# Optimization experiments

Measured on AMD Instinct MI355X. Metric: run time of the kernel, lower is better.

Reference implementation:

```python
import jax, jax.numpy as jnp
import numpy as np

B, S, D = 4, 4096, 256


def _complex_linear(x_r, x_i, w_r, w_i):
    # torch nn.Linear: y = x @ W.T ; complex mult: (Wr + i Wi)(xr + i xi)
    real = x_r @ w_r.T - x_i @ w_i.T
    imag = x_i @ w_r.T + x_r @ w_i.T
    return real, imag


def setup_inputs() -> dict:
    key = jax.random.key(0)
    ks = jax.random.split(key, 8)
    std = 1.0 / np.sqrt(D)  # ~ nn.Linear default init scale
    return {
        "query_real": jax.random.normal(ks[0], (B, S, D), jnp.float32),
        "query_imag": jax.random.normal(ks[1], (B, S, D), jnp.float32),
        "wq_real": jax.random.normal(ks[2], (D, D), jnp.float32) * std,
        "wq_imag": jax.random.normal(ks[3], (D, D), jnp.float32) * std,
        "wk_real": jax.random.normal(ks[4], (D, D), jnp.float32) * std,
        "wk_imag": jax.random.normal(ks[5], (D, D), jnp.float32) * std,
        "wv_real": jax.random.normal(ks[6], (D, D), jnp.float32) * std,
        "wv_imag": jax.random.normal(ks[7], (D, D), jnp.float32) * std,
    }


def reference(query_real, query_imag, wq_real, wq_imag, wk_real, wk_imag, wv_real, wv_imag):
    dim = query_real.shape[-1]
    scale = dim ** (-0.5)  # faithful: uses dim, not 2*dim

    q_r, q_i = _complex_linear(query_real, query_imag, wq_real, wq_imag)
    k_r, k_i = _complex_linear(query_real, query_imag, wk_real, wk_imag)
    v_r, v_i = _complex_linear(query_real, query_imag, wv_real, wv_imag)

    q_flat = jnp.concatenate([q_r, q_i], axis=-1)  # [B,S,2D]
    k_flat = jnp.concatenate([k_r, k_i], axis=-1)  # [B,S,2D]

    scores = jnp.einsum('bqd,bkd->bqk', q_flat, k_flat) * scale  # [B,S,S]
    attn = jax.nn.softmax(scores, axis=-1)

    out_r = jnp.einsum('bqk,bkd->bqd', attn, v_r)
    out_i = jnp.einsum('bqk,bkd->bqd', attn, v_i)
    return out_r, out_i, attn
```

## Files before the change

kernel.cpp:

```cpp
#include <hip/hip_runtime.h>
#include <hip/hip_fp16.h>

typedef _Float16 f16;
typedef _Float16 f16x8 __attribute__((ext_vector_type(8)));
typedef _Float16 f16x4 __attribute__((ext_vector_type(4)));
typedef float f32x4 __attribute__((ext_vector_type(4)));

#define AS1 __attribute__((address_space(1)))
#define AS3 __attribute__((address_space(3)))

__device__ __forceinline__ void g2l16(const void* g, void* l) {
  __builtin_amdgcn_global_load_lds((const AS1 void*)g, (AS3 void*)l, 16, 0, 0);
}

__device__ __forceinline__ void xcd_swz(int& bx, int& by, int& bz) {
  int gx = gridDim.x, gy = gridDim.y;
  int nwg = gx * gy * gridDim.z;
  int lin = (blockIdx.z * gy + blockIdx.y) * gx + blockIdx.x;
  int swz = (lin & 7) * (nwg >> 3) + (lin >> 3);
  bx = swz % gx;
  int t = swz / gx;
  by = t % gy;
  bz = t / gy;
}

__global__ __launch_bounds__(256) void build_x(const float* __restrict__ qr,
                                               const float* __restrict__ qi,
                                               f16* __restrict__ X) {
  long i = (long)blockIdx.x * 256 + threadIdx.x;
  long e = i * 4;
  int m = (int)(e >> 9);
  int k = (int)(e & 511);
  const float* src = (k < 256) ? (qr + (long)m * 256 + k)
                               : (qi + (long)m * 256 + (k - 256));
  float4 v = *(const float4*)src;
  f16x4 h = {(f16)v.x, (f16)v.y, (f16)v.z, (f16)v.w};
  *(f16x4*)(X + e) = h;
}

__global__ __launch_bounds__(256) void build_w(const float* __restrict__ wqr,
                                               const float* __restrict__ wqi,
                                               const float* __restrict__ wkr,
                                               const float* __restrict__ wki,
                                               const float* __restrict__ wvr,
                                               const float* __restrict__ wvi,
                                               f16* __restrict__ W) {
  long i = (long)blockIdx.x * 256 + threadIdx.x;
  long e = i * 4;
  int n = (int)(e >> 9);
  int k = (int)(e & 511);
  int sel = n >> 8;
  int row = n & 255;
  int k2 = k & 255;
  bool hi = (k >= 256);
  const float *Wr, *Wi;
  if ((sel >> 1) == 0)      { Wr = wqr; Wi = wqi; }
  else if ((sel >> 1) == 1) { Wr = wkr; Wi = wki; }
  else                      { Wr = wvr; Wi = wvi; }
  const float* src;
  float sgn = 1.0f;
  if ((sel & 1) == 0) {
    if (!hi) src = Wr + (long)row * 256 + k2;
    else   { src = Wi + (long)row * 256 + k2; sgn = -1.0f; }
  } else {
    if (!hi) src = Wi + (long)row * 256 + k2;
    else     src = Wr + (long)row * 256 + k2;
  }
  float4 v = *(const float4*)src;
  f16x4 h = {(f16)(sgn * v.x), (f16)(sgn * v.y), (f16)(sgn * v.z), (f16)(sgn * v.w)};
  *(f16x4*)(W + e) = h;
}

template <int MODE>
__global__ __launch_bounds__(256) void gemm_nt(const f16* __restrict__ A, int lda, long astr,
                                               const f16* __restrict__ B, int ldb, long bstr,
                                               int K, float scale,
                                               void* __restrict__ C0, long cstr,
                                               float2* __restrict__ stats) {
  __shared__ __align__(16) f16 As[128 * 64];
  __shared__ __align__(16) f16 Bs[128 * 64];
  int bx, by, bz;
  xcd_swz(bx, by, bz);
  const f16* Ab = A + (long)bz * astr;
  const f16* Bb = B + (long)bz * bstr;
  const int tid = threadIdx.x;
  const int wave = tid >> 6, lane = tid & 63;
  const int bm = by * 128, bn = bx * 128;
  const int wm = (wave >> 1) * 64, wn = (wave & 1) * 64;
  const int lr = lane & 15, lg = lane >> 4;

  const int srow = wave * 8 + (lane >> 3);
  const int sk = ((lane & 7) ^ (lane >> 3)) * 8;

  f32x4 acc[4][4] = {};

  for (int kt = 0; kt < K; kt += 64) {
#pragma unroll
    for (int it = 0; it < 4; ++it) {
      int r = srow + it * 32;
      g2l16(Ab + (long)(bm + r) * lda + kt + sk, (char*)As + it * 4096 + wave * 1024);
      g2l16(Bb + (long)(bn + r) * ldb + kt + sk, (char*)Bs + it * 4096 + wave * 1024);
    }
    __syncthreads();
#pragma unroll
    for (int kk = 0; kk < 2; ++kk) {
      f16x8 af[4], bf[4];
#pragma unroll
      for (int f = 0; f < 4; ++f) {
        int sw = ((kk * 4 + lg) ^ (lr & 7)) * 8;
        af[f] = *(const f16x8*)(As + (wm + f * 16 + lr) * 64 + sw);
        bf[f] = *(const f16x8*)(Bs + (wn + f * 16 + lr) * 64 + sw);
      }
#pragma unroll
      for (int fm = 0; fm < 4; ++fm)
#pragma unroll
        for (int fn = 0; fn < 4; ++fn)
          acc[fm][fn] = __builtin_amdgcn_mfma_f32_16x16x32_f16(af[fm], bf[fn], acc[fm][fn], 0, 0, 0);
    }
    __syncthreads();
  }

#pragma unroll
  for (int fm = 0; fm < 4; ++fm) {
#pragma unroll
    for (int fn = 0; fn < 4; ++fn) {
#pragma unroll
      for (int r = 0; r < 4; ++r) {
        int row = bm + wm + fm * 16 + lg * 4 + r;
        int col = bn + wn + fn * 16 + lr;
        float v = acc[fm][fn][r];
        if (MODE == 0) {
          ((f16*)C0)[(long)row * 1536 + col] = (f16)v;
        } else {
          ((f16*)C0)[(long)bz * cstr + (long)row * 4096 + col] = (f16)(v * scale);
        }
      }
    }
  }

  if (MODE == 1) {
    const int nt = bx * 2 + (wn >> 6);
#pragma unroll
    for (int fm = 0; fm < 4; ++fm) {
#pragma unroll
      for (int r = 0; r < 4; ++r) {
        float v0 = acc[fm][0][r] * scale, v1 = acc[fm][1][r] * scale;
        float v2 = acc[fm][2][r] * scale, v3 = acc[fm][3][r] * scale;
        float mt = fmaxf(fmaxf(v0, v1), fmaxf(v2, v3));
#pragma unroll
        for (int off = 8; off >= 1; off >>= 1) mt = fmaxf(mt, __shfl_xor(mt, off));
        float lt = __expf(v0 - mt) + __expf(v1 - mt) + __expf(v2 - mt) + __expf(v3 - mt);
#pragma unroll
        for (int off = 8; off >= 1; off >>= 1) lt += __shfl_xor(lt, off);
        if (lr == 0) {
          int row = bm + wm + fm * 16 + lg * 4 + r;
          stats[(long)nt * 16384 + (long)bz * 4096 + row] = make_float2(mt, lt);
        }
      }
    }
  }
}

__global__ __launch_bounds__(256) void build_vt(const f16* __restrict__ P,
                                                f16* __restrict__ VT) {
  __shared__ f16 t[64][66];
  const int tid = threadIdx.x;
  const long b = blockIdx.z;
  const f16* src = P + (b * 4096 + (long)blockIdx.x * 64) * 1536 + 1024 + blockIdx.y * 64;
#pragma unroll
  for (int it = 0; it < 16; ++it) {
    int lin = it * 256 + tid;
    int i = lin >> 6, j = lin & 63;
    t[i][j] = src[(long)i * 1536 + j];
  }
  __syncthreads();
  f16* dst = VT + (b * 512 + (long)blockIdx.y * 64) * 4096 + blockIdx.x * 64;
#pragma unroll
  for (int it = 0; it < 16; ++it) {
    int lin = it * 256 + tid;
    int i = lin >> 6, j = lin & 63;
    dst[(long)i * 4096 + j] = t[j][i];
  }
}

__global__ __launch_bounds__(256) void merge_stats(const float2* __restrict__ stats,
                                                   float2* __restrict__ ml) {
  long row = (long)blockIdx.x * 256 + threadIdx.x;
  float m = -1e30f;
#pragma unroll 8
  for (int i = 0; i < 64; ++i) m = fmaxf(m, stats[i * 16384 + row].x);
  float l = 0.0f;
#pragma unroll 8
  for (int i = 0; i < 64; ++i) {
    float2 s = stats[i * 16384 + row];
    l += s.y * __expf(s.x - m);
  }
  ml[row] = make_float2(m, l);
}

__global__ __launch_bounds__(512, 4) void pv_fused2(const float2* __restrict__ ml,
                                                    const f16* __restrict__ S16,
                                                    const f16* __restrict__ VT,
                                                    float* __restrict__ attn,
                                                    float* __restrict__ outR,
                                                    float* __restrict__ outI) {
  __shared__ __align__(16) f16 Ps0[64 * 64];
  __shared__ __align__(16) f16 Ps1[64 * 64];
  __shared__ __align__(16) f16 Bs0[256 * 64];
  __shared__ __align__(16) f16 Bs1[256 * 64];
  int lin = blockIdx.x;
  int swz = (lin & 7) * 64 + (lin >> 3);
  int b = swz >> 7;
  int rem = swz & 127;
  int rt = rem >> 1, ch = rem & 1;
  const int bm = rt * 64;
  const int c0 = ch * 256;

  const int tid = threadIdx.x;
  const int wave = tid >> 6, lane = tid & 63;
  const int wm2 = (wave >> 2) * 32;
  const int wn2 = (wave & 3) * 64;
  const int lr = lane & 15, lg = lane >> 4;

  const int prow = tid >> 3;
  const int pc8 = tid & 7;
  const int vrow = wave * 8 + (lane >> 3);
  const int vsw = ((lane & 7) ^ ((lane >> 3) & 7)) * 8;
  float2 mlv = ml[(long)b * 4096 + bm + prow];
  const float mrow = mlv.x;
  const float invl = 1.0f / mlv.y;
  const bool writer = (ch == 0);

  const f16* Sb = S16 + ((long)(b * 4096 + bm + prow)) * 4096 + pc8 * 8;
  float* Ab = attn + ((long)(b * 4096 + bm + prow)) * 4096 + pc8 * 8;
  const f16* Vb = VT + (long)(b * 512 + c0) * 4096;
  const int pslot = (pc8 ^ (prow & 7)) * 8;

  f32x4 acc[2][4] = {};
  f16x8 sc0, sc1;

#define PV_EXP(SC, PSBUF, KT)                                               \
  {                                                                         \
    float p[8];                                                             \
    _Pragma("unroll") for (int j = 0; j < 8; ++j)                           \
      p[j] = __expf((float)SC[j] - mrow) * invl;                            \
    if (writer) {                                                           \
      float4 w0 = {p[0], p[1], p[2], p[3]};                                 \
      float4 w1 = {p[4], p[5], p[6], p[7]};                                 \
      *(float4*)(Ab + (KT)) = w0;                                           \
      *(float4*)(Ab + (KT) + 4) = w1;                                       \
    }                                                                       \
    f16x8 h = {(f16)p[0], (f16)p[1], (f16)p[2], (f16)p[3],                  \
               (f16)p[4], (f16)p[5], (f16)p[6], (f16)p[7]};                 \
    *(f16x8*)(PSBUF + prow * 64 + pslot) = h;                               \
  }

#define PV_MFMA(PSBUF, BSBUF)                                               \
  {                                                                         \
    _Pragma("unroll")                                                       \
    for (int kk = 0; kk < 2; ++kk) {                                        \
      f16x8 af[2];                                                          \
      _Pragma("unroll")                                                     \
      for (int fm = 0; fm < 2; ++fm)                                        \
        af[fm] = *(const f16x8*)(PSBUF + (wm2 + fm * 16 + lr) * 64 +        \
                                 ((kk * 4 + lg) ^ (lr & 7)) * 8);           \
      f16x8 bf[4];                                                          \
      _Pragma("unroll")                                                     \
      for (int f = 0; f < 4; ++f)                                           \
        bf[f] = *(const f16x8*)(BSBUF + (wn2 + f * 16 + lr) * 64 +          \
                                ((kk * 4 + lg) ^ (lr & 7)) * 8);            \
      _Pragma("unroll")                                                     \
      for (int fm = 0; fm < 2; ++fm)                                        \
        _Pragma("unroll")                                                   \
        for (int f = 0; f < 4; ++f)                                         \
          acc[fm][f] = __builtin_amdgcn_mfma_f32_16x16x32_f16(              \
              af[fm], bf[f], acc[fm][f], 0, 0, 0);                          \
    }                                                                       \
  }

#define PV_G2L(BSBUF, KT)                                                   \
  {                                                                         \
    _Pragma("unroll")                                                       \
    for (int i = 0; i < 4; ++i)                                             \
      g2l16(Vb + (long)(i * 64 + vrow) * 4096 + (KT) + vsw,                 \
            (char*)BSBUF + i * 8192 + wave * 1024);                         \
  }

#define PV_STEP(T, SA, SB, PSC, BSC, PSN, BSN)                              \
  {                                                                         \
    if ((T) + 2 < 64) SA = *(const f16x8*)(Sb + ((T) + 2) * 64);            \
    if ((T) + 1 < 64) PV_G2L(BSN, ((T) + 1) * 64)                           \
    PV_MFMA(PSC, BSC)                                                       \
    if ((T) + 1 < 64) PV_EXP(SB, PSN, ((T) + 1) * 64)                       \
    __syncthreads();                                                        \
  }

  sc0 = *(const f16x8*)(Sb + 0);
  sc1 = *(const f16x8*)(Sb + 64);
  PV_G2L(Bs0, 0)
  PV_EXP(sc0, Ps0, 0)
  __syncthreads();

  for (int t2 = 0; t2 < 64; t2 += 2) {
    PV_STEP(t2,     sc0, sc1, Ps0, Bs0, Ps1, Bs1)
    PV_STEP(t2 + 1, sc1, sc0, Ps1, Bs1, Ps0, Bs0)
  }
#undef PV_STEP
#undef PV_G2L
#undef PV_MFMA
#undef PV_EXP

  float* outp = ch ? outI : outR;
#pragma unroll
  for (int fm = 0; fm < 2; ++fm)
#pragma unroll
    for (int f = 0; f < 4; ++f)
#pragma unroll
      for (int r = 0; r < 4; ++r) {
        int row = bm + wm2 + fm * 16 + lg * 4 + r;
        int col = wn2 + f * 16 + lr;
        outp[((long)b * 4096 + row) * 256 + col] = acc[fm][f][r];
      }
}

extern "C" void kernel_launch(void* const* d_in, const int* in_sizes, int n_in,
                              void* d_out, int out_size, void* d_ws, size_t ws_size,
                              hipStream_t stream) {
  const float* qr  = (const float*)d_in[0];
  const float* qi  = (const float*)d_in[1];
  const float* wqr = (const float*)d_in[2];
  const float* wqi = (const float*)d_in[3];
  const float* wkr = (const float*)d_in[4];
  const float* wki = (const float*)d_in[5];
  const float* wvr = (const float*)d_in[6];
  const float* wvi = (const float*)d_in[7];

  float* outR = (float*)d_out;
  float* outI = outR + (size_t)4 * 4096 * 256;
  float* attn = outI + (size_t)4 * 4096 * 256;

  const size_t offX  = 0;
  const size_t offW  = offX + (size_t)16384 * 512 * 2;
  const size_t offP  = offW + (size_t)1536 * 512 * 2;
  const size_t offVT = offP + (size_t)16384 * 1536 * 2;
  const size_t offS  = offVT + (size_t)4 * 512 * 4096 * 2;

  char* ws = (char*)d_ws;
  f16* X   = (f16*)(ws + offX);
  f16* W   = (f16*)(ws + offW);
  f16* P   = (f16*)(ws + offP);
  f16* VT  = (f16*)(ws + offVT);
  f16* S16 = (f16*)(ws + offS);
  float2* stats = (float2*)X;
  float2* ml    = (float2*)W;

  build_x<<<8192, 256, 0, stream>>>(qr, qi, X);
  build_w<<<768, 256, 0, stream>>>(wqr, wqi, wkr, wki, wvr, wvi, W);

  gemm_nt<0><<<dim3(12, 128, 1), 256, 0, stream>>>(X, 512, 0L, W, 512, 0L, 512, 1.0f,
                                                   (void*)P, 0L, nullptr);

  build_vt<<<dim3(64, 8, 4), 256, 0, stream>>>(P, VT);

  gemm_nt<1><<<dim3(32, 32, 4), 256, 0, stream>>>(P, 1536, (long)4096 * 1536,
                                                  P + 512, 1536, (long)4096 * 1536,
                                                  512, 0.0625f,
                                                  (void*)S16, (long)4096 * 4096, stats);

  merge_stats<<<64, 256, 0, stream>>>(stats, ml);

  pv_fused2<<<512, 512, 0, stream>>>(ml, S16, VT, attn, outR, outI);
}
```

Measured before the change: 375.6 us.

## Enlarge GEMM tiles to 256x128 and halve PV k-step for higher occupancy

The NT GEMM kernel now runs 512 threads per block on a 256x128 output tile instead of 256 threads on 128x128. This halves the grid and reuses each loaded B tile across twice as many rows. The fused softmax-PV kernel switches from 64-wide to 32-wide K slices with smaller LDS buffers, a new swizzle and an occupancy hint of 6. The aim is to fit more resident blocks and hide latency, at the cost of twice as many barrier-separated steps and narrower per-thread attn stores.

```diff
diff --git a/kernel.cpp b/kernel.cpp
--- a/kernel.cpp
+++ b/kernel.cpp
@@ -72,12 +72,12 @@
 }
 
 template <int MODE>
-__global__ __launch_bounds__(256) void gemm_nt(const f16* __restrict__ A, int lda, long astr,
-                                               const f16* __restrict__ B, int ldb, long bstr,
-                                               int K, float scale,
-                                               void* __restrict__ C0, long cstr,
-                                               float2* __restrict__ stats) {
-  __shared__ __align__(16) f16 As[128 * 64];
+__global__ __launch_bounds__(512, 4) void gemm_nt(const f16* __restrict__ A, int lda, long astr,
+                                                  const f16* __restrict__ B, int ldb, long bstr,
+                                                  int K, float scale,
+                                                  void* __restrict__ C0, long cstr,
+                                                  float2* __restrict__ stats) {
+  __shared__ __align__(16) f16 As[256 * 64];
   __shared__ __align__(16) f16 Bs[128 * 64];
   int bx, by, bz;
   xcd_swz(bx, by, bz);
@@ -85,7 +85,7 @@
   const f16* Bb = B + (long)bz * bstr;
   const int tid = threadIdx.x;
   const int wave = tid >> 6, lane = tid & 63;
-  const int bm = by * 128, bn = bx * 128;
+  const int bm = by * 256, bn = bx * 128;
   const int wm = (wave >> 1) * 64, wn = (wave & 1) * 64;
   const int lr = lane & 15, lg = lane >> 4;
 
@@ -96,11 +96,13 @@
 
   for (int kt = 0; kt < K; kt += 64) {
 #pragma unroll
-    for (int it = 0; it < 4; ++it) {
-      int r = srow + it * 32;
-      g2l16(Ab + (long)(bm + r) * lda + kt + sk, (char*)As + it * 4096 + wave * 1024);
-      g2l16(Bb + (long)(bn + r) * ldb + kt + sk, (char*)Bs + it * 4096 + wave * 1024);
-    }
+    for (int it = 0; it < 4; ++it)
+      g2l16(Ab + (long)(bm + srow + it * 64) * lda + kt + sk,
+            (char*)As + it * 8192 + wave * 1024);
+#pragma unroll
+    for (int it = 0; it < 2; ++it)
+      g2l16(Bb + (long)(bn + srow + it * 64) * ldb + kt + sk,
+            (char*)Bs + it * 8192 + wave * 1024);
     __syncthreads();
 #pragma unroll
     for (int kk = 0; kk < 2; ++kk) {
@@ -198,16 +200,16 @@
   ml[row] = make_float2(m, l);
 }
 
-__global__ __launch_bounds__(512, 4) void pv_fused2(const float2* __restrict__ ml,
+__global__ __launch_bounds__(512, 6) void pv_fused3(const float2* __restrict__ ml,
                                                     const f16* __restrict__ S16,
                                                     const f16* __restrict__ VT,
                                                     float* __restrict__ attn,
                                                     float* __restrict__ outR,
                                                     float* __restrict__ outI) {
-  __shared__ __align__(16) f16 Ps0[64 * 64];
-  __shared__ __align__(16) f16 Ps1[64 * 64];
-  __shared__ __align__(16) f16 Bs0[256 * 64];
-  __shared__ __align__(16) f16 Bs1[256 * 64];
+  __shared__ __align__(16) f16 Ps0[64 * 32];
+  __shared__ __align__(16) f16 Ps1[64 * 32];
+  __shared__ __align__(16) f16 Bs0[256 * 32];
+  __shared__ __align__(16) f16 Bs1[256 * 32];
   int lin = blockIdx.x;
   int swz = (lin & 7) * 64 + (lin >> 3);
   int b = swz >> 7;
@@ -221,87 +223,80 @@
   const int wm2 = (wave >> 2) * 32;
   const int wn2 = (wave & 3) * 64;
   const int lr = lane & 15, lg = lane >> 4;
+  const int koff = (lg ^ ((lr >> 1) & 3)) * 8;
 
   const int prow = tid >> 3;
-  const int pc8 = tid & 7;
-  const int vrow = wave * 8 + (lane >> 3);
-  const int vsw = ((lane & 7) ^ ((lane >> 3) & 7)) * 8;
+  const int pc4 = tid & 7;
+  const int vsw = ((lane & 3) ^ ((lane >> 3) & 3)) * 8;
   float2 mlv = ml[(long)b * 4096 + bm + prow];
   const float mrow = mlv.x;
   const float invl = 1.0f / mlv.y;
   const bool writer = (ch == 0);
 
-  const f16* Sb = S16 + ((long)(b * 4096 + bm + prow)) * 4096 + pc8 * 8;
-  float* Ab = attn + ((long)(b * 4096 + bm + prow)) * 4096 + pc8 * 8;
+  const f16* Sb = S16 + ((long)(b * 4096 + bm + prow)) * 4096 + pc4 * 4;
+  float* Ab = attn + ((long)(b * 4096 + bm + prow)) * 4096 + pc4 * 4;
   const f16* Vb = VT + (long)(b * 512 + c0) * 4096;
-  const int pslot = (pc8 ^ (prow & 7)) * 8;
+  const int pslot = (((pc4 >> 1) ^ ((prow >> 1) & 3)) * 8) + (pc4 & 1) * 4;
 
   f32x4 acc[2][4] = {};
-  f16x8 sc0, sc1;
+  f16x4 sc0, sc1;
 
 #define PV_EXP(SC, PSBUF, KT)                                               \
   {                                                                         \
-    float p[8];                                                             \
-    _Pragma("unroll") for (int j = 0; j < 8; ++j)                           \
-      p[j] = __expf((float)SC[j] - mrow) * invl;                            \
+    float p0 = __expf((float)SC[0] - mrow) * invl;                          \
+    float p1 = __expf((float)SC[1] - mrow) * invl;                          \
+    float p2 = __expf((float)SC[2] - mrow) * invl;                          \
+    float p3 = __expf((float)SC[3] - mrow) * invl;                          \
     if (writer) {                                                           \
-      float4 w0 = {p[0], p[1], p[2], p[3]};                                 \
-      float4 w1 = {p[4], p[5], p[6], p[7]};                                 \
+      float4 w0 = {p0, p1, p2, p3};                                         \
       *(float4*)(Ab + (KT)) = w0;                                           \
-      *(float4*)(Ab + (KT) + 4) = w1;                                       \
     }                                                                       \
-    f16x8 h = {(f16)p[0], (f16)p[1], (f16)p[2], (f16)p[3],                  \
-               (f16)p[4], (f16)p[5], (f16)p[6], (f16)p[7]};                 \
-    *(f16x8*)(PSBUF + prow * 64 + pslot) = h;                               \
+    f16x4 h = {(f16)p0, (f16)p1, (f16)p2, (f16)p3};                         \
+    *(f16x4*)(PSBUF + prow * 32 + pslot) = h;                               \
   }
 
 #define PV_MFMA(PSBUF, BSBUF)                                               \
   {                                                                         \
+    f16x8 af[2];                                                            \
     _Pragma("unroll")                                                       \
-    for (int kk = 0; kk < 2; ++kk) {                                        \
-      f16x8 af[2];                                                          \
-      _Pragma("unroll")                                                     \
-      for (int fm = 0; fm < 2; ++fm)                                        \
-        af[fm] = *(const f16x8*)(PSBUF + (wm2 + fm * 16 + lr) * 64 +        \
-                                 ((kk * 4 + lg) ^ (lr & 7)) * 8);           \
-      f16x8 bf[4];                                                          \
+    for (int fm = 0; fm < 2; ++fm)                                          \
+      af[fm] = *(const f16x8*)(PSBUF + (wm2 + fm * 16 + lr) * 32 + koff);   \
+    f16x8 bf[4];                                                            \
+    _Pragma("unroll")                                                       \
+    for (int f = 0; f < 4; ++f)                                             \
+      bf[f] = *(const f16x8*)(BSBUF + (wn2 + f * 16 + lr) * 32 + koff);     \
+    _Pragma("unroll")                                                       \
+    for (int fm = 0; fm < 2; ++fm)                                          \
       _Pragma("unroll")                                                     \
       for (int f = 0; f < 4; ++f)                                           \
-        bf[f] = *(const f16x8*)(BSBUF + (wn2 + f * 16 + lr) * 64 +          \
-                                ((kk * 4 + lg) ^ (lr & 7)) * 8);            \
-      _Pragma("unroll")                                                     \
-      for (int fm = 0; fm < 2; ++fm)                                        \
-        _Pragma("unroll")                                                   \
-        for (int f = 0; f < 4; ++f)                                         \
-          acc[fm][f] = __builtin_amdgcn_mfma_f32_16x16x32_f16(              \
-              af[fm], bf[f], acc[fm][f], 0, 0, 0);                          \
-    }                                                                       \
+        acc[fm][f] = __builtin_amdgcn_mfma_f32_16x16x32_f16(                \
+            af[fm], bf[f], acc[fm][f], 0, 0, 0);                            \
   }
 
 #define PV_G2L(BSBUF, KT)                                                   \
   {                                                                         \
     _Pragma("unroll")                                                       \
-    for (int i = 0; i < 4; ++i)                                             \
-      g2l16(Vb + (long)(i * 64 + vrow) * 4096 + (KT) + vsw,                 \
-            (char*)BSBUF + i * 8192 + wave * 1024);                         \
+    for (int j = 0; j < 2; ++j)                                             \
+      g2l16(Vb + (long)(j * 128 + wave * 16 + (lane >> 2)) * 4096 + (KT) + vsw, \
+            (char*)BSBUF + j * 8192 + wave * 1024);                         \
   }
 
 #define PV_STEP(T, SA, SB, PSC, BSC, PSN, BSN)                              \
   {                                                                         \
-    if ((T) + 2 < 64) SA = *(const f16x8*)(Sb + ((T) + 2) * 64);            \
-    if ((T) + 1 < 64) PV_G2L(BSN, ((T) + 1) * 64)                           \
+    if ((T) + 2 < 128) SA = *(const f16x4*)(Sb + ((T) + 2) * 32);           \
+    if ((T) + 1 < 128) PV_G2L(BSN, ((T) + 1) * 32)                          \
     PV_MFMA(PSC, BSC)                                                       \
-    if ((T) + 1 < 64) PV_EXP(SB, PSN, ((T) + 1) * 64)                       \
+    if ((T) + 1 < 128) PV_EXP(SB, PSN, ((T) + 1) * 32)                      \
     __syncthreads();                                                        \
   }
 
-  sc0 = *(const f16x8*)(Sb + 0);
-  sc1 = *(const f16x8*)(Sb + 64);
+  sc0 = *(const f16x4*)(Sb + 0);
+  sc1 = *(const f16x4*)(Sb + 32);
   PV_G2L(Bs0, 0)
   PV_EXP(sc0, Ps0, 0)
   __syncthreads();
 
-  for (int t2 = 0; t2 < 64; t2 += 2) {
+  for (int t2 = 0; t2 < 128; t2 += 2) {
     PV_STEP(t2,     sc0, sc1, Ps0, Bs0, Ps1, Bs1)
     PV_STEP(t2 + 1, sc1, sc0, Ps1, Bs1, Ps0, Bs0)
   }
@@ -357,17 +352,17 @@
   build_x<<<8192, 256, 0, stream>>>(qr, qi, X);
   build_w<<<768, 256, 0, stream>>>(wqr, wqi, wkr, wki, wvr, wvi, W);
 
-  gemm_nt<0><<<dim3(12, 128, 1), 256, 0, stream>>>(X, 512, 0L, W, 512, 0L, 512, 1.0f,
-                                                   (void*)P, 0L, nullptr);
+  gemm_nt<0><<<dim3(12, 64, 1), 512, 0, stream>>>(X, 512, 0L, W, 512, 0L, 512, 1.0f,
+                                                  (void*)P, 0L, nullptr);
 
   build_vt<<<dim3(64, 8, 4), 256, 0, stream>>>(P, VT);
 
-  gemm_nt<1><<<dim3(32, 32, 4), 256, 0, stream>>>(P, 1536, (long)4096 * 1536,
+  gemm_nt<1><<<dim3(32, 16, 4), 512, 0, stream>>>(P, 1536, (long)4096 * 1536,
                                                   P + 512, 1536, (long)4096 * 1536,
                                                   512, 0.0625f,
                                                   (void*)S16, (long)4096 * 4096, stats);
 
   merge_stats<<<64, 256, 0, stream>>>(stats, ml);
 
-  pv_fused2<<<512, 512, 0, stream>>>(ml, S16, VT, attn, outR, outI);
-}
+  pv_fused3<<<512, 512, 0, stream>>>(ml, S16, VT, attn, outR, outI);
+}
```

Result: no change. 376.6 us (+0.3%).

## Triple-buffer PV pipeline, split attn stores across halves, enlarge GEMM tiles

Applied to the files above, without the earlier changes.

The fused softmax-PV kernel moves from double to triple buffering. It prefetches V tiles two steps ahead with explicit vmcnt waits in place of full syncthreads, and raises wave priority around the MFMA blocks. The attn-probability writes now alternate between the two column-half blocks instead of all going to one, which balances the store traffic. The QKV and QK^T GEMMs use 256x128 tiles with 512 threads to improve operand reuse, at the cost of more LDS and registers per block and fewer blocks in the grid.

```diff
diff --git a/kernel.cpp b/kernel.cpp
--- a/kernel.cpp
+++ b/kernel.cpp
@@ -72,12 +72,12 @@
 }
 
 template <int MODE>
-__global__ __launch_bounds__(256) void gemm_nt(const f16* __restrict__ A, int lda, long astr,
-                                               const f16* __restrict__ B, int ldb, long bstr,
-                                               int K, float scale,
-                                               void* __restrict__ C0, long cstr,
-                                               float2* __restrict__ stats) {
-  __shared__ __align__(16) f16 As[128 * 64];
+__global__ __launch_bounds__(512, 4) void gemm_nt(const f16* __restrict__ A, int lda, long astr,
+                                                  const f16* __restrict__ B, int ldb, long bstr,
+                                                  int K, float scale,
+                                                  void* __restrict__ C0, long cstr,
+                                                  float2* __restrict__ stats) {
+  __shared__ __align__(16) f16 As[256 * 64];
   __shared__ __align__(16) f16 Bs[128 * 64];
   int bx, by, bz;
   xcd_swz(bx, by, bz);
@@ -85,7 +85,7 @@
   const f16* Bb = B + (long)bz * bstr;
   const int tid = threadIdx.x;
   const int wave = tid >> 6, lane = tid & 63;
-  const int bm = by * 128, bn = bx * 128;
+  const int bm = by * 256, bn = bx * 128;
   const int wm = (wave >> 1) * 64, wn = (wave & 1) * 64;
   const int lr = lane & 15, lg = lane >> 4;
 
@@ -96,11 +96,13 @@
 
   for (int kt = 0; kt < K; kt += 64) {
 #pragma unroll
-    for (int it = 0; it < 4; ++it) {
-      int r = srow + it * 32;
-      g2l16(Ab + (long)(bm + r) * lda + kt + sk, (char*)As + it * 4096 + wave * 1024);
-      g2l16(Bb + (long)(bn + r) * ldb + kt + sk, (char*)Bs + it * 4096 + wave * 1024);
-    }
+    for (int it = 0; it < 4; ++it)
+      g2l16(Ab + (long)(bm + srow + it * 64) * lda + kt + sk,
+            (char*)As + it * 8192 + wave * 1024);
+#pragma unroll
+    for (int it = 0; it < 2; ++it)
+      g2l16(Bb + (long)(bn + srow + it * 64) * ldb + kt + sk,
+            (char*)Bs + it * 8192 + wave * 1024);
     __syncthreads();
 #pragma unroll
     for (int kk = 0; kk < 2; ++kk) {
@@ -198,16 +200,18 @@
   ml[row] = make_float2(m, l);
 }
 
-__global__ __launch_bounds__(512, 4) void pv_fused2(const float2* __restrict__ ml,
-                                                    const f16* __restrict__ S16,
-                                                    const f16* __restrict__ VT,
-                                                    float* __restrict__ attn,
-                                                    float* __restrict__ outR,
-                                                    float* __restrict__ outI) {
+__global__ __launch_bounds__(512) void pv_fused4(const float2* __restrict__ ml,
+                                                 const f16* __restrict__ S16,
+                                                 const f16* __restrict__ VT,
+                                                 float* __restrict__ attn,
+                                                 float* __restrict__ outR,
+                                                 float* __restrict__ outI) {
   __shared__ __align__(16) f16 Ps0[64 * 64];
   __shared__ __align__(16) f16 Ps1[64 * 64];
+  __shared__ __align__(16) f16 Ps2[64 * 64];
   __shared__ __align__(16) f16 Bs0[256 * 64];
   __shared__ __align__(16) f16 Bs1[256 * 64];
+  __shared__ __align__(16) f16 Bs2[256 * 64];
   int lin = blockIdx.x;
   int swz = (lin & 7) * 64 + (lin >> 3);
   int b = swz >> 7;
@@ -229,7 +233,6 @@
   float2 mlv = ml[(long)b * 4096 + bm + prow];
   const float mrow = mlv.x;
   const float invl = 1.0f / mlv.y;
-  const bool writer = (ch == 0);
 
   const f16* Sb = S16 + ((long)(b * 4096 + bm + prow)) * 4096 + pc8 * 8;
   float* Ab = attn + ((long)(b * 4096 + bm + prow)) * 4096 + pc8 * 8;
@@ -237,14 +240,22 @@
   const int pslot = (pc8 ^ (prow & 7)) * 8;
 
   f32x4 acc[2][4] = {};
-  f16x8 sc0, sc1;
-
-#define PV_EXP(SC, PSBUF, KT)                                               \
+  f16x8 s0, s1, s2, sini;
+
+#define PV_G2L(BSBUF, KT)                                                   \
+  {                                                                         \
+    _Pragma("unroll")                                                       \
+    for (int i = 0; i < 4; ++i)                                             \
+      g2l16(Vb + (long)(i * 64 + vrow) * 4096 + (KT) + vsw,                 \
+            (char*)BSBUF + i * 8192 + wave * 1024);                         \
+  }
+
+#define PV_EXP(SC, PSBUF, KT, PAR)                                          \
   {                                                                         \
     float p[8];                                                             \
     _Pragma("unroll") for (int j = 0; j < 8; ++j)                           \
       p[j] = __expf((float)SC[j] - mrow) * invl;                            \
-    if (writer) {                                                           \
+    if ((PAR) == ch) {                                                      \
       float4 w0 = {p[0], p[1], p[2], p[3]};                                 \
       float4 w1 = {p[4], p[5], p[6], p[7]};                                 \
       *(float4*)(Ab + (KT)) = w0;                                           \
@@ -257,6 +268,7 @@
 
 #define PV_MFMA(PSBUF, BSBUF)                                               \
   {                                                                         \
+    __builtin_amdgcn_s_setprio(1);                                          \
     _Pragma("unroll")                                                       \
     for (int kk = 0; kk < 2; ++kk) {                                        \
       f16x8 af[2];                                                          \
@@ -276,39 +288,66 @@
           acc[fm][f] = __builtin_amdgcn_mfma_f32_16x16x32_f16(              \
               af[fm], bf[f], acc[fm][f], 0, 0, 0);                          \
     }                                                                       \
-  }
-
-#define PV_G2L(BSBUF, KT)                                                   \
+    __builtin_amdgcn_s_setprio(0);                                          \
+  }
+
+#define PV_SYNC(N)                                                          \
+  asm volatile("s_waitcnt vmcnt(" #N ")" ::: "memory");                     \
+  asm volatile("s_waitcnt lgkmcnt(0)" ::: "memory");                        \
+  __builtin_amdgcn_s_barrier();                                             \
+  __builtin_amdgcn_sched_barrier(0);
+
+#define PV_TILE(T, BCUR, BPRE, PCUR, PNXT, SCONS, SLOAD)                    \
   {                                                                         \
-    _Pragma("unroll")                                                       \
-    for (int i = 0; i < 4; ++i)                                             \
-      g2l16(Vb + (long)(i * 64 + vrow) * 4096 + (KT) + vsw,                 \
-            (char*)BSBUF + i * 8192 + wave * 1024);                         \
-  }
-
-#define PV_STEP(T, SA, SB, PSC, BSC, PSN, BSN)                              \
-  {                                                                         \
-    if ((T) + 2 < 64) SA = *(const f16x8*)(Sb + ((T) + 2) * 64);            \
-    if ((T) + 1 < 64) PV_G2L(BSN, ((T) + 1) * 64)                           \
-    PV_MFMA(PSC, BSC)                                                       \
-    if ((T) + 1 < 64) PV_EXP(SB, PSN, ((T) + 1) * 64)                       \
-    __syncthreads();                                                        \
-  }
-
-  sc0 = *(const f16x8*)(Sb + 0);
-  sc1 = *(const f16x8*)(Sb + 64);
+    PV_G2L(BPRE, ((T) + 2) * 64)                                            \
+    SLOAD = *(const f16x8*)(Sb + ((T) + 3) * 64);                           \
+    PV_EXP(SCONS, PNXT, ((T) + 1) * 64, (((T) + 1) & 1))                    \
+    PV_MFMA(PCUR, BCUR)                                                     \
+    PV_SYNC(8)                                                              \
+  }
+
   PV_G2L(Bs0, 0)
-  PV_EXP(sc0, Ps0, 0)
-  __syncthreads();
-
-  for (int t2 = 0; t2 < 64; t2 += 2) {
-    PV_STEP(t2,     sc0, sc1, Ps0, Bs0, Ps1, Bs1)
-    PV_STEP(t2 + 1, sc1, sc0, Ps1, Bs1, Ps0, Bs0)
-  }
-#undef PV_STEP
-#undef PV_G2L
+  PV_G2L(Bs1, 64)
+  sini = *(const f16x8*)(Sb + 0);
+  s1 = *(const f16x8*)(Sb + 64);
+  s2 = *(const f16x8*)(Sb + 128);
+  PV_EXP(sini, Ps0, 0, 0)
+  PV_SYNC(7)
+
+  for (int tb = 0; tb < 60; tb += 6) {
+    PV_TILE(tb + 0, Bs0, Bs2, Ps0, Ps1, s1, s0)
+    PV_TILE(tb + 1, Bs1, Bs0, Ps1, Ps2, s2, s1)
+    PV_TILE(tb + 2, Bs2, Bs1, Ps2, Ps0, s0, s2)
+    PV_TILE(tb + 3, Bs0, Bs2, Ps0, Ps1, s1, s0)
+    PV_TILE(tb + 4, Bs1, Bs0, Ps1, Ps2, s2, s1)
+    PV_TILE(tb + 5, Bs2, Bs1, Ps2, Ps0, s0, s2)
+  }
+
+  {
+    PV_G2L(Bs2, 62 * 64)
+    s0 = *(const f16x8*)(Sb + 63 * 64);
+    PV_EXP(s1, Ps1, 61 * 64, 1)
+    PV_MFMA(Ps0, Bs0)
+    PV_SYNC(8)
+  }
+  {
+    PV_G2L(Bs0, 63 * 64)
+    PV_EXP(s2, Ps2, 62 * 64, 0)
+    PV_MFMA(Ps1, Bs1)
+    PV_SYNC(7)
+  }
+  {
+    PV_EXP(s0, Ps0, 63 * 64, 1)
+    PV_MFMA(Ps2, Bs2)
+    PV_SYNC(2)
+  }
+  PV_MFMA(Ps0, Bs0)
+
+#undef PV_TILE
+#undef PV_SYNC
 #undef PV_MFMA
 #undef PV_EXP
+#undef PV_G2L
 
   float* outp = ch ? outI : outR;
 #pragma unroll
@@ -357,17 +396,17 @@
   build_x<<<8192, 256, 0, stream>>>(qr, qi, X);
   build_w<<<768, 256, 0, stream>>>(wqr, wqi, wkr, wki, wvr, wvi, W);
 
-  gemm_nt<0><<<dim3(12, 128, 1), 256, 0, stream>>>(X, 512, 0L, W, 512, 0L, 512, 1.0f,
-                                                   (void*)P, 0L, nullptr);
+  gemm_nt<0><<<dim3(12, 64, 1), 512, 0, stream>>>(X, 512, 0L, W, 512, 0L, 512, 1.0f,
+                                                  (void*)P, 0L, nullptr);
 
   build_vt<<<dim3(64, 8, 4), 256, 0, stream>>>(P, VT);
 
-  gemm_nt<1><<<dim3(32, 32, 4), 256, 0, stream>>>(P, 1536, (long)4096 * 1536,
+  gemm_nt<1><<<dim3(32, 16, 4), 512, 0, stream>>>(P, 1536, (long)4096 * 1536,
                                                   P + 512, 1536, (long)4096 * 1536,
                                                   512, 0.0625f,
                                                   (void*)S16, (long)4096 * 4096, stats);
 
   merge_stats<<<64, 256, 0, stream>>>(stats, ml);
 
-  pv_fused2<<<512, 512, 0, stream>>>(ml, S16, VT, attn, outR, outI);
-}
+  pv_fused4<<<512, 512, 0, stream>>>(ml, S16, VT, attn, outR, outI);
+}
```

Measured after the change: 367.7 us. 2.1% less time.
